# Kernel tuning notes

Hardware: AMD Instinct MI355X
Metric: run time of the kernel (lower is better)

## Reference

```python
import jax, jax.numpy as jnp
import numpy as np

NHEAD = 8
LN_EPS = 1e-5


def _layernorm(x, g, b):
    mu = jnp.mean(x, -1, keepdims=True)
    var = jnp.mean((x - mu) ** 2, -1, keepdims=True)
    return (x - mu) / jnp.sqrt(var + LN_EPS) * g + b


def _sparse_attn(q, k, v, P):
    # Topology: P queries attend to P keys; G queries attend to P keys + self.
    # q,k,v: [B,H,L,dh], keys/values restricted to pcpt block [B,H,P,dh]
    dh = q.shape[-1]
    scale = 1.0 / jnp.sqrt(jnp.asarray(dh, q.dtype))
    kp, vp = k[:, :, :P], v[:, :, :P]
    S = jnp.einsum('bhld,bhpd->bhlp', q, kp) * scale  # [B,H,L,P]
    # pcpt queries: plain softmax over P keys
    out_p = jnp.einsum('bhqp,bhpd->bhqd', jax.nn.softmax(S[:, :, :P], axis=-1), vp)
    # gen queries: P keys + own diagonal key
    qg, kg, vg = q[:, :, P:], k[:, :, P:], v[:, :, P:]
    Sg = S[:, :, P:]                                   # [B,H,G,P]
    dlog = jnp.sum(qg * kg, -1) * scale                # [B,H,G] diagonal logits
    m = jnp.maximum(jnp.max(Sg, -1), dlog)
    eg = jnp.exp(Sg - m[..., None])
    ed = jnp.exp(dlog - m)
    den = jnp.sum(eg, -1) + ed
    out_g = (jnp.einsum('bhgp,bhpd->bhgd', eg, vp) + ed[..., None] * vg) / den[..., None]
    return jnp.concatenate([out_p, out_g], axis=2)     # [B,H,L,dh]


def _forward(pcpt, gen, Wqkv, bqkv, Wo, bo, W1, b1, W2, b2, g1, beta1, g2, beta2):
    P = pcpt.shape[1]
    x = jnp.concatenate([pcpt, gen], axis=1)           # [B,L,d]
    B, L, d = x.shape
    dh = d // NHEAD
    for i in range(Wqkv.shape[0]):  # post-norm layers
        qkv = (x @ Wqkv[i] + bqkv[i]).reshape(B, L, 3, NHEAD, dh)
        q = jnp.transpose(qkv[:, :, 0], (0, 2, 1, 3))
        k = jnp.transpose(qkv[:, :, 1], (0, 2, 1, 3))
        v = jnp.transpose(qkv[:, :, 2], (0, 2, 1, 3))
        a = _sparse_attn(q, k, v, P)
        a = jnp.transpose(a, (0, 2, 1, 3)).reshape(B, L, d)
        a = a @ Wo[i] + bo[i]
        x = _layernorm(x + a, g1[i], beta1[i])
        h = jax.nn.relu(x @ W1[i] + b1[i]) @ W2[i] + b2[i]
        x = _layernorm(x + h, g2[i], beta2[i])
    return x


def setup_inputs() -> dict:
    key = jax.random.key(0)
    ks = jax.random.split(key, 16)
    B, P, G, d, ff, Lyr = 4, 1024, 1024, 512, 2048, 4
    s = 0.02
    f32 = jnp.float32
    return {
        'pcpt_total_embs': jax.random.normal(ks[0], (B, P, d), f32),
        'gen_total_embs': jax.random.normal(ks[1], (B, G, d), f32),
        'src_key_padding_mask': jnp.zeros((B, P + G), bool),
        'Wqkv': jax.random.normal(ks[2], (Lyr, d, 3 * d), f32) * s,
        'bqkv': jnp.zeros((Lyr, 3 * d), f32),
        'Wo': jax.random.normal(ks[3], (Lyr, d, d), f32) * s,
        'bo': jnp.zeros((Lyr, d), f32),
        'W1': jax.random.normal(ks[4], (Lyr, d, ff), f32) * s,
        'b1': jnp.zeros((Lyr, ff), f32),
        'W2': jax.random.normal(ks[5], (Lyr, ff, d), f32) * s,
        'b2': jnp.zeros((Lyr, d), f32),
        'g1': jnp.ones((Lyr, d), f32),
        'beta1': jnp.zeros((Lyr, d), f32),
        'g2': jnp.ones((Lyr, d), f32),
        'beta2': jnp.zeros((Lyr, d), f32),
    }


def reference(pcpt_total_embs, gen_total_embs, src_key_padding_mask, Wqkv, bqkv, Wo, bo, W1, b1, W2, b2, g1, beta1, g2, beta2):
    P = pcpt_total_embs.shape[1]
    x = _forward(pcpt_total_embs, gen_total_embs, Wqkv, bqkv, Wo, bo, W1, b1, W2, b2, g1, beta1, g2, beta2)
    return x[:, :P], x[:, P:]
```

## Files before the change

kernel.cpp:

```cpp
#include <hip/hip_runtime.h>
#include <hip/hip_bf16.h>

#define B_ 4
#define P_ 1024
#define G_ 1024
#define L_ 2048
#define D_ 512
#define FF_ 2048
#define H_ 8
#define DH_ 64
#define LAYERS_ 4
#define LN_EPS_ 1e-5f

typedef __attribute__((ext_vector_type(8))) short bf16x8;
typedef __attribute__((ext_vector_type(4))) float f32x4;

__device__ __forceinline__ ushort f2b(float f) {
  unsigned u = __float_as_uint(f);
  unsigned r = (u + 0x7fffu + ((u >> 16) & 1u)) >> 16;
  return (ushort)r;
}
__device__ __forceinline__ float b2f(ushort u) {
  return __uint_as_float(((unsigned)u) << 16);
}

__device__ __forceinline__ void gld16(const ushort* g, ushort* l) {
  __builtin_amdgcn_global_load_lds(
      (const __attribute__((address_space(1))) void*)g,
      (__attribute__((address_space(3))) void*)l, 16, 0, 0);
}

__global__ __launch_bounds__(256) void concat_kernel(const float* __restrict__ p,
    const float* __restrict__ g, float* __restrict__ x, ushort* __restrict__ xb)
{
  const int LD4 = L_*D_/4, PD4 = P_*D_/4;
  int i = blockIdx.x*256 + threadIdx.x;
  int b = i / LD4, r = i - b*LD4;
  float4 v;
  if (r < PD4) v = ((const float4*)p)[(size_t)b*PD4 + r];
  else         v = ((const float4*)g)[(size_t)b*PD4 + (r-PD4)];
  ((float4*)x)[i] = v;
  ushort4 h; h.x=f2b(v.x); h.y=f2b(v.y); h.z=f2b(v.z); h.w=f2b(v.w);
  ((ushort4*)xb)[i] = h;
}

__global__ __launch_bounds__(256) void writeout_kernel(const float* __restrict__ x,
    float* __restrict__ out)
{
  const int LD4 = L_*D_/4, PD4 = P_*D_/4, HALF = B_*PD4;
  int i = blockIdx.x*256 + threadIdx.x;
  int half = (i >= HALF) ? 1 : 0;
  int r = i - half*HALF;
  int b = r / PD4, q = r - b*PD4;
  ((float4*)out)[i] = ((const float4*)x)[(size_t)b*LD4 + half*PD4 + q];
}

__global__ __launch_bounds__(256) void wconv_kernel(const float* __restrict__ src,
    ushort* __restrict__ dst, int K, int N)
{
  __shared__ float tile[32][33];
  int n0 = blockIdx.x*32, k0 = blockIdx.y*32, l = blockIdx.z;
  src += (size_t)l*K*N; dst += (size_t)l*K*N;
  int tx = threadIdx.x & 31, ty = threadIdx.x >> 5;
  #pragma unroll
  for (int u=0;u<4;++u) tile[ty+8*u][tx] = src[(size_t)(k0+ty+8*u)*N + n0+tx];
  __syncthreads();
  #pragma unroll
  for (int u=0;u<4;++u) dst[(size_t)(n0+ty+8*u)*K + k0+tx] = f2b(tile[tx][ty+8*u]);
}

template<int BN_, int RELU, int RES, int OUTBF>
__global__ __launch_bounds__(256) void mgemm(
    const ushort* __restrict__ A, const ushort* __restrict__ Bt,
    const float* __restrict__ bias, const float* __restrict__ res,
    void* __restrict__ Cout, int M, int N, int K)
{
  constexpr int MI = (BN_ == 128) ? 4 : 2;
  constexpr int BL = BN_ / 32;
  __shared__ ushort As[128*64];
  __shared__ ushort Bs[BN_*64];
  int t = threadIdx.x;
  int lane = t & 63, w = t >> 6;
  int wm = (BN_ == 128) ? (w >> 1) * 64 : w * 32;
  int wn = (BN_ == 128) ? (w & 1) * 64 : 0;
  int m0 = blockIdx.x * 128, n0 = blockIdx.y * BN_;

  f32x4 acc[MI][4] = {};

  int rbase = t >> 3;
  int cch   = (t & 7) ^ ((t >> 3) & 7);
  const ushort* Ag = A  + (size_t)(m0 + rbase)*K + cch*8;
  const ushort* Bg = Bt + (size_t)(n0 + rbase)*K + cch*8;
  ushort* Asl = As + t*8;
  ushort* Bsl = Bs + t*8;
  const size_t rowK32 = (size_t)32 * K;

  int fr = lane & 15, fq = lane >> 4;
  int swr[2];
  swr[0] = ((0*4 + fq) ^ (fr & 7)) * 8;
  swr[1] = ((1*4 + fq) ^ (fr & 7)) * 8;
  const ushort* Ard = As + (wm + fr)*64;
  const ushort* Brd = Bs + (wn + fr)*64;

  for (int k0 = 0; k0 < K; k0 += 64) {
    __syncthreads();
    #pragma unroll
    for (int L = 0; L < 4; ++L)  gld16(Ag + L*rowK32, Asl + L*2048);
    #pragma unroll
    for (int L = 0; L < BL; ++L) gld16(Bg + L*rowK32, Bsl + L*2048);
    Ag += 64; Bg += 64;
    __syncthreads();
    #pragma unroll
    for (int s = 0; s < 2; ++s) {
      int sw = swr[s];
      bf16x8 af[MI], bfr[4];
      #pragma unroll
      for (int i=0;i<MI;++i) af[i]  = *(const bf16x8*)(Ard + i*16*64 + sw);
      #pragma unroll
      for (int j=0;j<4;++j)  bfr[j] = *(const bf16x8*)(Brd + j*16*64 + sw);
      #pragma unroll
      for (int i=0;i<MI;++i)
        #pragma unroll
        for (int j=0;j<4;++j)
          acc[i][j] = __builtin_amdgcn_mfma_f32_16x16x32_bf16(af[i], bfr[j], acc[i][j], 0, 0, 0);
    }
  }

  int ncol = lane & 15;
  int rquad = (lane >> 4) * 4;
  #pragma unroll
  for (int j=0;j<4;++j) {
    int n = n0 + wn + j*16 + ncol;
    float bv = bias[n];
    #pragma unroll
    for (int i=0;i<MI;++i) {
      int mbase = m0 + wm + i*16 + rquad;
      #pragma unroll
      for (int r=0;r<4;++r) {
        int m = mbase + r;
        float c = acc[i][j][r] + bv;
        if (RES) c += res[(size_t)m*N + n];
        if (RELU) c = fmaxf(c, 0.f);
        if (OUTBF) ((ushort*)Cout)[(size_t)m*N + n] = f2b(c);
        else       ((float*)Cout)[(size_t)m*N + n] = c;
      }
    }
  }
}

__global__ __launch_bounds__(256) void mgemm_qkv(
    const ushort* __restrict__ A,
    const ushort* __restrict__ Bt,
    const float* __restrict__ bias,
    ushort* __restrict__ qb,
    ushort* __restrict__ kb,
    ushort* __restrict__ vtb)
{
  const int K = D_;
  __shared__ ushort As[128*64];
  __shared__ ushort Bs[128*64];
  int t = threadIdx.x;
  int lane = t & 63, w = t >> 6;
  int wm = (w >> 1) * 64, wn = (w & 1) * 64;
  int m0 = blockIdx.x * 128, n0 = blockIdx.y * 128;

  f32x4 acc[4][4] = {};

  int rbase = t >> 3;
  int cch   = (t & 7) ^ ((t >> 3) & 7);
  const ushort* Ag = A  + (size_t)(m0 + rbase)*K + cch*8;
  const ushort* Bg = Bt + (size_t)(n0 + rbase)*K + cch*8;
  ushort* Asl = As + t*8;
  ushort* Bsl = Bs + t*8;
  const size_t rowK32 = (size_t)32 * K;

  int fr = lane & 15, fq = lane >> 4;
  int swr[2];
  swr[0] = ((0*4 + fq) ^ (fr & 7)) * 8;
  swr[1] = ((1*4 + fq) ^ (fr & 7)) * 8;
  const ushort* Ard = As + (wm + fr)*64;
  const ushort* Brd = Bs + (wn + fr)*64;

  for (int k0 = 0; k0 < K; k0 += 64) {
    __syncthreads();
    #pragma unroll
    for (int L = 0; L < 4; ++L) gld16(Ag + L*rowK32, Asl + L*2048);
    #pragma unroll
    for (int L = 0; L < 4; ++L) gld16(Bg + L*rowK32, Bsl + L*2048);
    Ag += 64; Bg += 64;
    __syncthreads();
    #pragma unroll
    for (int s = 0; s < 2; ++s) {
      int sw = swr[s];
      bf16x8 af[4], bfr[4];
      #pragma unroll
      for (int i=0;i<4;++i) af[i]  = *(const bf16x8*)(Ard + i*16*64 + sw);
      #pragma unroll
      for (int j=0;j<4;++j) bfr[j] = *(const bf16x8*)(Brd + j*16*64 + sw);
      #pragma unroll
      for (int i=0;i<4;++i)
        #pragma unroll
        for (int j=0;j<4;++j)
          acc[i][j] = __builtin_amdgcn_mfma_f32_16x16x32_bf16(af[i], bfr[j], acc[i][j], 0, 0, 0);
    }
  }

  int ncol = lane & 15;
  int rquad = (lane >> 4) * 4;
  #pragma unroll
  for (int j=0;j<4;++j) {
    int n = n0 + wn + j*16 + ncol;
    float bv = bias[n];
    int part = n >> 9;
    int wi = n & 511;
    int h = wi >> 6, d = wi & 63;
    #pragma unroll
    for (int i=0;i<4;++i) {
      int mbase = m0 + wm + i*16 + rquad;
      #pragma unroll
      for (int r=0;r<4;++r) {
        int m = mbase + r;
        int b = m >> 11, l = m & 2047;
        int bh = b*H_ + h;
        float cv = acc[i][j][r] + bv;
        if (part == 0) cv *= 0.125f;
        ushort c = f2b(cv);
        if (part == 0)      qb[((size_t)bh*L_ + l)*DH_ + d] = c;
        else if (part == 1) kb[((size_t)bh*L_ + l)*DH_ + d] = c;
        else                vtb[((size_t)bh*DH_ + d)*L_ + l] = c;
      }
    }
  }
}

__global__ __launch_bounds__(256) void attn_mfma(
    const ushort* __restrict__ qb, const ushort* __restrict__ kb,
    const ushort* __restrict__ vtb, ushort* __restrict__ outa)
{
  __shared__ ushort Ks[2][64*64];
  __shared__ ushort Vts[2][64*64];
  __shared__ ushort Ps[8*16*72];

  int t = threadIdx.x;
  int lane = t & 63, w = t >> 6;
  int qt = blockIdx.x & 15;
  int h  = (blockIdx.x >> 4) & 7;
  int b  = blockIdx.x >> 7;
  int l0 = qt * 128;
  bool isgen = (l0 >= P_);
  int bh = b*H_ + h;

  const ushort* qg  = qb  + ((size_t)bh*L_ + l0)*DH_;
  const ushort* kgb = kb  + (size_t)bh*L_*DH_;
  const ushort* vtg = vtb + (size_t)bh*DH_*L_;

  int sr  = t >> 3;
  int scg = (t & 7) * 8;
  int scs = ((t & 7) ^ (sr & 7)) * 8;

  int fr = lane & 15, fq = lane >> 4;
  int swz0 = ((0*4 + fq) ^ (fr & 7)) * 8;
  int swz1 = ((1*4 + fq) ^ (fr & 7)) * 8;

  bf16x8 qf[2][2];
  #pragma unroll
  for (int i=0;i<2;++i) {
    qf[i][0] = *(const bf16x8*)(qg + (size_t)(w*32 + i*16 + fr)*DH_ + fq*8);
    qf[i][1] = *(const bf16x8*)(qg + (size_t)(w*32 + i*16 + fr)*DH_ + 32 + fq*8);
  }

  float den[2][4] = {};
  f32x4 o[2][4] = {};
  ushort* Pw0 = Ps + (w*2 + 0)*16*72;
  ushort* Pw1 = Ps + (w*2 + 1)*16*72;

  {
    uint4 a0 = *(const uint4*)(kgb + (size_t)sr*DH_ + scg);
    uint4 a1 = *(const uint4*)(kgb + (size_t)(sr+32)*DH_ + scg);
    uint4 a2 = *(const uint4*)(vtg + (size_t)sr*L_ + scg);
    uint4 a3 = *(const uint4*)(vtg + (size_t)(sr+32)*L_ + scg);
    *(uint4*)(&Ks[0][sr*64 + scs])       = a0;
    *(uint4*)(&Ks[0][(sr+32)*64 + scs])  = a1;
    *(uint4*)(&Vts[0][sr*64 + scs])      = a2;
    *(uint4*)(&Vts[0][(sr+32)*64 + scs]) = a3;
  }
  uint4 pk0 = *(const uint4*)(kgb + (size_t)(64+sr)*DH_ + scg);
  uint4 pk1 = *(const uint4*)(kgb + (size_t)(64+sr+32)*DH_ + scg);
  uint4 pv0 = *(const uint4*)(vtg + (size_t)sr*L_ + 64 + scg);
  uint4 pv1 = *(const uint4*)(vtg + (size_t)(sr+32)*L_ + 64 + scg);
  __syncthreads();

  for (int kt = 0; kt < 16; ++kt) {
    const ushort* Kc = &Ks[kt & 1][0];
    const ushort* Vc = &Vts[kt & 1][0];
    if (kt < 15) {
      ushort* Kn = &Ks[(kt+1) & 1][0];
      ushort* Vn = &Vts[(kt+1) & 1][0];
      *(uint4*)(Kn + sr*64 + scs)      = pk0;
      *(uint4*)(Kn + (sr+32)*64 + scs) = pk1;
      *(uint4*)(Vn + sr*64 + scs)      = pv0;
      *(uint4*)(Vn + (sr+32)*64 + scs) = pv1;
    }
    if (kt < 14) {
      int p2 = (kt + 2) * 64;
      pk0 = *(const uint4*)(kgb + (size_t)(p2+sr)*DH_ + scg);
      pk1 = *(const uint4*)(kgb + (size_t)(p2+sr+32)*DH_ + scg);
      pv0 = *(const uint4*)(vtg + (size_t)sr*L_ + p2 + scg);
      pv1 = *(const uint4*)(vtg + (size_t)(sr+32)*L_ + p2 + scg);
    }

    f32x4 sc4[2][4] = {};
    __builtin_amdgcn_s_setprio(1);
    #pragma unroll
    for (int s=0;s<2;++s) {
      int sw = s ? swz1 : swz0;
      #pragma unroll
      for (int j=0;j<4;++j) {
        bf16x8 kf = *(const bf16x8*)(Kc + (j*16 + fr)*64 + sw);
        sc4[0][j] = __builtin_amdgcn_mfma_f32_16x16x32_bf16(qf[0][s], kf, sc4[0][j], 0, 0, 0);
        sc4[1][j] = __builtin_amdgcn_mfma_f32_16x16x32_bf16(qf[1][s], kf, sc4[1][j], 0, 0, 0);
      }
    }
    __builtin_amdgcn_s_setprio(0);

    #pragma unroll
    for (int i=0;i<2;++i) {
      ushort* Pw = i ? Pw1 : Pw0;
      #pragma unroll
      for (int r=0;r<4;++r) {
        float e0 = __expf(sc4[i][0][r]);
        float e1 = __expf(sc4[i][1][r]);
        float e2 = __expf(sc4[i][2][r]);
        float e3 = __expf(sc4[i][3][r]);
        den[i][r] += (e0+e1) + (e2+e3);
        Pw[(fq*4+r)*72 +  0 + fr] = (ushort)(__float_as_uint(e0) >> 16);
        Pw[(fq*4+r)*72 + 16 + fr] = (ushort)(__float_as_uint(e1) >> 16);
        Pw[(fq*4+r)*72 + 32 + fr] = (ushort)(__float_as_uint(e2) >> 16);
        Pw[(fq*4+r)*72 + 48 + fr] = (ushort)(__float_as_uint(e3) >> 16);
      }
    }
    asm volatile("s_waitcnt lgkmcnt(0)" ::: "memory");

    __builtin_amdgcn_s_setprio(1);
    #pragma unroll
    for (int s=0;s<2;++s) {
      int sw = s ? swz1 : swz0;
      bf16x8 pf0 = *(const bf16x8*)(Pw0 + fr*72 + s*32 + fq*8);
      bf16x8 pf1 = *(const bf16x8*)(Pw1 + fr*72 + s*32 + fq*8);
      #pragma unroll
      for (int j=0;j<4;++j) {
        bf16x8 vf = *(const bf16x8*)(Vc + (j*16 + fr)*64 + sw);
        o[0][j] = __builtin_amdgcn_mfma_f32_16x16x32_bf16(pf0, vf, o[0][j], 0, 0, 0);
        o[1][j] = __builtin_amdgcn_mfma_f32_16x16x32_bf16(pf1, vf, o[1][j], 0, 0, 0);
      }
    }
    __builtin_amdgcn_s_setprio(0);
    __syncthreads();
  }

  #pragma unroll
  for (int i=0;i<2;++i)
    #pragma unroll
    for (int r=0;r<4;++r) {
      float d = den[i][r];
      d += __shfl_xor(d, 1, 16);
      d += __shfl_xor(d, 2, 16);
      d += __shfl_xor(d, 4, 16);
      d += __shfl_xor(d, 8, 16);
      den[i][r] = d;
    }

  if (isgen) {
    #pragma unroll
    for (int i=0;i<2;++i) {
      int base = l0 + w*32 + i*16;
      f32x4 dsc = {};
      {
        bf16x8 kd0 = *(const bf16x8*)(kgb + (size_t)(base + fr)*DH_ + fq*8);
        dsc = __builtin_amdgcn_mfma_f32_16x16x32_bf16(qf[i][0], kd0, dsc, 0, 0, 0);
        bf16x8 kd1 = *(const bf16x8*)(kgb + (size_t)(base + fr)*DH_ + 32 + fq*8);
        dsc = __builtin_amdgcn_mfma_f32_16x16x32_bf16(qf[i][1], kd1, dsc, 0, 0, 0);
      }
      #pragma unroll
      for (int r=0;r<4;++r) {
        int m = fq*4 + r;
        float dl = __shfl(dsc[r], fq*16 + m);
        float ed = __expf(dl);
        den[i][r] += ed;
        int l = base + m;
        #pragma unroll
        for (int j=0;j<4;++j) {
          float vv = b2f(vtg[(size_t)(j*16 + fr)*L_ + l]);
          o[i][j][r] += ed*vv;
        }
      }
    }
  }

  #pragma unroll
  for (int i=0;i<2;++i)
    #pragma unroll
    for (int r=0;r<4;++r) {
      float inv = 1.f / den[i][r];
      int l = l0 + w*32 + i*16 + fq*4 + r;
      #pragma unroll
      for (int j=0;j<4;++j)
        outa[((size_t)b*L_ + l)*D_ + h*DH_ + j*16 + fr] = f2b(o[i][j][r]*inv);
    }
}

__global__ __launch_bounds__(64) void ln_kernel(const float* __restrict__ y,
    const float* __restrict__ gw, const float* __restrict__ bw,
    float* __restrict__ x, ushort* __restrict__ xb)
{
  int row = blockIdx.x, t = threadIdx.x;
  const float4* yr = (const float4*)(y + (size_t)row*D_);
  float4 v0 = yr[t], v1 = yr[t+64];
  float s = v0.x+v0.y+v0.z+v0.w + v1.x+v1.y+v1.z+v1.w;
  for (int off=32; off>0; off>>=1) s += __shfl_down(s, off, 64);
  s = __shfl(s, 0, 64);
  float mu = s * (1.f/D_);
  float dx;
  float q = 0.f;
  dx=v0.x-mu; q+=dx*dx; dx=v0.y-mu; q+=dx*dx; dx=v0.z-mu; q+=dx*dx; dx=v0.w-mu; q+=dx*dx;
  dx=v1.x-mu; q+=dx*dx; dx=v1.y-mu; q+=dx*dx; dx=v1.z-mu; q+=dx*dx; dx=v1.w-mu; q+=dx*dx;
  for (int off=32; off>0; off>>=1) q += __shfl_down(q, off, 64);
  q = __shfl(q, 0, 64);
  float rinv = rsqrtf(q*(1.f/D_) + LN_EPS_);
  const float4* g4 = (const float4*)gw;
  const float4* b4 = (const float4*)bw;
  float4 gv0=g4[t], gv1=g4[t+64], bv0=b4[t], bv1=b4[t+64];
  float4 o0, o1;
  o0.x=(v0.x-mu)*rinv*gv0.x+bv0.x; o0.y=(v0.y-mu)*rinv*gv0.y+bv0.y;
  o0.z=(v0.z-mu)*rinv*gv0.z+bv0.z; o0.w=(v0.w-mu)*rinv*gv0.w+bv0.w;
  o1.x=(v1.x-mu)*rinv*gv1.x+bv1.x; o1.y=(v1.y-mu)*rinv*gv1.y+bv1.y;
  o1.z=(v1.z-mu)*rinv*gv1.z+bv1.z; o1.w=(v1.w-mu)*rinv*gv1.w+bv1.w;
  float4* xr = (float4*)(x + (size_t)row*D_);
  xr[t]=o0; xr[t+64]=o1;
  ushort4 h0, h1;
  h0.x=f2b(o0.x); h0.y=f2b(o0.y); h0.z=f2b(o0.z); h0.w=f2b(o0.w);
  h1.x=f2b(o1.x); h1.y=f2b(o1.y); h1.z=f2b(o1.z); h1.w=f2b(o1.w);
  ushort4* xbr = (ushort4*)(xb + (size_t)row*D_);
  xbr[t]=h0; xbr[t+64]=h1;
}

extern "C" void kernel_launch(void* const* d_in, const int* in_sizes, int n_in,
                              void* d_out, int out_size, void* d_ws, size_t ws_size,
                              hipStream_t stream) {
  const float* pcpt = (const float*)d_in[0];
  const float* gen  = (const float*)d_in[1];
  const float* Wqkv = (const float*)d_in[3];
  const float* bqkv = (const float*)d_in[4];
  const float* Wo   = (const float*)d_in[5];
  const float* bo   = (const float*)d_in[6];
  const float* W1   = (const float*)d_in[7];
  const float* b1   = (const float*)d_in[8];
  const float* W2   = (const float*)d_in[9];
  const float* b2   = (const float*)d_in[10];
  const float* g1   = (const float*)d_in[11];
  const float* be1  = (const float*)d_in[12];
  const float* g2   = (const float*)d_in[13];
  const float* be2  = (const float*)d_in[14];
  float* out = (float*)d_out;

  const size_t XD  = (size_t)B_*L_*D_;
  const size_t HKV = (size_t)B_*H_*L_*DH_;
  const size_t HFF = (size_t)B_*L_*FF_;

  float*  xbuf = (float*)d_ws;
  ushort* xbf  = (ushort*)(xbuf + XD);
  ushort* region = xbf + XD;
  ushort* qb  = region;
  ushort* kb  = region + HKV;
  ushort* vtb = region + 2*HKV;
  ushort* hbf = region;
  ushort* abf = region + HFF;
  ushort* wb  = abf + XD;
  ushort* wqkv_b = wb;
  ushort* wo_b   = wqkv_b + (size_t)4*3*D_*D_;
  ushort* w1_b   = wo_b   + (size_t)4*D_*D_;
  ushort* w2_b   = w1_b   + (size_t)4*FF_*D_;
  float*  ybuf = out;

  const int M = B_*L_;

  wconv_kernel<<<dim3(3*D_/32, D_/32, 4), 256, 0, stream>>>(Wqkv, wqkv_b, D_, 3*D_);
  wconv_kernel<<<dim3(D_/32,   D_/32, 4), 256, 0, stream>>>(Wo,   wo_b,   D_, D_);
  wconv_kernel<<<dim3(FF_/32,  D_/32, 4), 256, 0, stream>>>(W1,   w1_b,   D_, FF_);
  wconv_kernel<<<dim3(D_/32,  FF_/32, 4), 256, 0, stream>>>(W2,   w2_b,   FF_, D_);

  concat_kernel<<<4096, 256, 0, stream>>>(pcpt, gen, xbuf, xbf);

  for (int i = 0; i < LAYERS_; ++i) {
    const ushort* wqkv_i = wqkv_b + (size_t)i*3*D_*D_;
    const ushort* wo_i   = wo_b   + (size_t)i*D_*D_;
    const ushort* w1_i   = w1_b   + (size_t)i*FF_*D_;
    const ushort* w2_i   = w2_b   + (size_t)i*D_*FF_;
    const float* bqkv_i = bqkv + (size_t)i*3*D_;
    const float* bo_i   = bo   + (size_t)i*D_;
    const float* b1_i   = b1   + (size_t)i*FF_;
    const float* b2_i   = b2   + (size_t)i*D_;
    const float* g1_i   = g1   + (size_t)i*D_;
    const float* be1_i  = be1  + (size_t)i*D_;
    const float* g2_i   = g2   + (size_t)i*D_;
    const float* be2_i  = be2  + (size_t)i*D_;

    mgemm_qkv<<<dim3(M/128, 3*D_/128), 256, 0, stream>>>(
        xbf, wqkv_i, bqkv_i, qb, kb, vtb);

    attn_mfma<<<B_*H_*(L_/128), 256, 0, stream>>>(qb, kb, vtb, abf);

    mgemm<64,0,1,0><<<dim3(M/128, D_/64), 256, 0, stream>>>(
        abf, wo_i, bo_i, xbuf, ybuf, M, D_, D_);

    ln_kernel<<<M, 64, 0, stream>>>(ybuf, g1_i, be1_i, xbuf, xbf);

    mgemm<128,1,0,1><<<dim3(M/128, FF_/128), 256, 0, stream>>>(
        xbf, w1_i, b1_i, nullptr, hbf, M, FF_, D_);

    mgemm<64,0,1,0><<<dim3(M/128, D_/64), 256, 0, stream>>>(
        hbf, w2_i, b2_i, xbuf, ybuf, M, D_, FF_);

    ln_kernel<<<M, 64, 0, stream>>>(ybuf, g2_i, be2_i, xbuf, xbf);
  }

  writeout_kernel<<<4096, 256, 0, stream>>>(xbuf, out);
}
```

Baseline: 798.0 us.

## Double-buffer LDS tiles in GEMM kernels to overlap global loads with MFMA

Both the generic GEMM and the QKV GEMM now keep two LDS buffers for the A and B tiles. The next K-tile is issued via direct global-to-LDS loads before computing on the current one, with a single waitcnt and barrier per iteration instead of two barriers. The aim is to hide global memory latency behind MFMA work. In exchange LDS use per block doubles (up to 64KB), which may lower occupancy.

```diff
diff --git a/kernel.cpp b/kernel.cpp
--- a/kernel.cpp
+++ b/kernel.cpp
@@ -77,8 +77,8 @@
 {
   constexpr int MI = (BN_ == 128) ? 4 : 2;
   constexpr int BL = BN_ / 32;
-  __shared__ ushort As[128*64];
-  __shared__ ushort Bs[BN_*64];
+  __shared__ ushort As[2*128*64];
+  __shared__ ushort Bs[2*BN_*64];
   int t = threadIdx.x;
   int lane = t & 63, w = t >> 6;
   int wm = (BN_ == 128) ? (w >> 1) * 64 : w * 32;
@@ -91,25 +91,39 @@
   int cch   = (t & 7) ^ ((t >> 3) & 7);
   const ushort* Ag = A  + (size_t)(m0 + rbase)*K + cch*8;
   const ushort* Bg = Bt + (size_t)(n0 + rbase)*K + cch*8;
-  ushort* Asl = As + t*8;
-  ushort* Bsl = Bs + t*8;
+  ushort* Asl0 = As + t*8;
+  ushort* Asl1 = As + 128*64 + t*8;
+  ushort* Bsl0 = Bs + t*8;
+  ushort* Bsl1 = Bs + BN_*64 + t*8;
   const size_t rowK32 = (size_t)32 * K;
 
   int fr = lane & 15, fq = lane >> 4;
   int swr[2];
   swr[0] = ((0*4 + fq) ^ (fr & 7)) * 8;
   swr[1] = ((1*4 + fq) ^ (fr & 7)) * 8;
-  const ushort* Ard = As + (wm + fr)*64;
-  const ushort* Brd = Bs + (wn + fr)*64;
-
-  for (int k0 = 0; k0 < K; k0 += 64) {
-    __syncthreads();
-    #pragma unroll
-    for (int L = 0; L < 4; ++L)  gld16(Ag + L*rowK32, Asl + L*2048);
-    #pragma unroll
-    for (int L = 0; L < BL; ++L) gld16(Bg + L*rowK32, Bsl + L*2048);
-    Ag += 64; Bg += 64;
-    __syncthreads();
+
+  #pragma unroll
+  for (int L = 0; L < 4; ++L)  gld16(Ag + L*rowK32, Asl0 + L*2048);
+  #pragma unroll
+  for (int L = 0; L < BL; ++L) gld16(Bg + L*rowK32, Bsl0 + L*2048);
+
+  const int NT = K >> 6;
+  for (int tt = 0; tt < NT; ++tt) {
+    asm volatile("s_waitcnt vmcnt(0)" ::: "memory");
+    __builtin_amdgcn_s_barrier();
+    __builtin_amdgcn_sched_barrier(0);
+    if (tt + 1 < NT) {
+      const ushort* Agn = Ag + (size_t)(tt+1)*64;
+      const ushort* Bgn = Bg + (size_t)(tt+1)*64;
+      ushort* Ad = (tt & 1) ? Asl0 : Asl1;
+      ushort* Bd = (tt & 1) ? Bsl0 : Bsl1;
+      #pragma unroll
+      for (int L = 0; L < 4; ++L)  gld16(Agn + L*rowK32, Ad + L*2048);
+      #pragma unroll
+      for (int L = 0; L < BL; ++L) gld16(Bgn + L*rowK32, Bd + L*2048);
+    }
+    const ushort* Ard = ((tt & 1) ? As + 128*64 : As) + (wm + fr)*64;
+    const ushort* Brd = ((tt & 1) ? Bs + BN_*64 : Bs) + (wn + fr)*64;
     #pragma unroll
     for (int s = 0; s < 2; ++s) {
       int sw = swr[s];
@@ -157,8 +171,8 @@
     ushort* __restrict__ vtb)
 {
   const int K = D_;
-  __shared__ ushort As[128*64];
-  __shared__ ushort Bs[128*64];
+  __shared__ ushort As[2*128*64];
+  __shared__ ushort Bs[2*128*64];
   int t = threadIdx.x;
   int lane = t & 63, w = t >> 6;
   int wm = (w >> 1) * 64, wn = (w & 1) * 64;
@@ -170,25 +184,39 @@
   int cch   = (t & 7) ^ ((t >> 3) & 7);
   const ushort* Ag = A  + (size_t)(m0 + rbase)*K + cch*8;
   const ushort* Bg = Bt + (size_t)(n0 + rbase)*K + cch*8;
-  ushort* Asl = As + t*8;
-  ushort* Bsl = Bs + t*8;
+  ushort* Asl0 = As + t*8;
+  ushort* Asl1 = As + 128*64 + t*8;
+  ushort* Bsl0 = Bs + t*8;
+  ushort* Bsl1 = Bs + 128*64 + t*8;
   const size_t rowK32 = (size_t)32 * K;
 
   int fr = lane & 15, fq = lane >> 4;
   int swr[2];
   swr[0] = ((0*4 + fq) ^ (fr & 7)) * 8;
   swr[1] = ((1*4 + fq) ^ (fr & 7)) * 8;
-  const ushort* Ard = As + (wm + fr)*64;
-  const ushort* Brd = Bs + (wn + fr)*64;
-
-  for (int k0 = 0; k0 < K; k0 += 64) {
-    __syncthreads();
-    #pragma unroll
-    for (int L = 0; L < 4; ++L) gld16(Ag + L*rowK32, Asl + L*2048);
-    #pragma unroll
-    for (int L = 0; L < 4; ++L) gld16(Bg + L*rowK32, Bsl + L*2048);
-    Ag += 64; Bg += 64;
-    __syncthreads();
+
+  #pragma unroll
+  for (int L = 0; L < 4; ++L) gld16(Ag + L*rowK32, Asl0 + L*2048);
+  #pragma unroll
+  for (int L = 0; L < 4; ++L) gld16(Bg + L*rowK32, Bsl0 + L*2048);
+
+  const int NT = K >> 6;
+  for (int tt = 0; tt < NT; ++tt) {
+    asm volatile("s_waitcnt vmcnt(0)" ::: "memory");
+    __builtin_amdgcn_s_barrier();
+    __builtin_amdgcn_sched_barrier(0);
+    if (tt + 1 < NT) {
+      const ushort* Agn = Ag + (size_t)(tt+1)*64;
+      const ushort* Bgn = Bg + (size_t)(tt+1)*64;
+      ushort* Ad = (tt & 1) ? Asl0 : Asl1;
+      ushort* Bd = (tt & 1) ? Bsl0 : Bsl1;
+      #pragma unroll
+      for (int L = 0; L < 4; ++L) gld16(Agn + L*rowK32, Ad + L*2048);
+      #pragma unroll
+      for (int L = 0; L < 4; ++L) gld16(Bgn + L*rowK32, Bd + L*2048);
+    }
+    const ushort* Ard = ((tt & 1) ? As + 128*64 : As) + (wm + fr)*64;
+    const ushort* Brd = ((tt & 1) ? Bs + 128*64 : Bs) + (wn + fr)*64;
     #pragma unroll
     for (int s = 0; s < 2; ++s) {
       int sw = swr[s];
```

After: 782.7 us. Within noise of the previous version (-1.9%).
